# Performance work log

Measured on AMD Instinct MI355X. Metric: run time of the kernel, lower is better.

The kernel has to match this reference:

```python
import jax, jax.numpy as jnp
import numpy as np

N_LOC, N_EVT, E = 100000, 200000, 1000000
F_LOC, F_EVT, H = 128, 128, 64


def setup_inputs() -> dict:
    key = jax.random.key(0)
    ks = jax.random.split(key, 12)
    s = lambda k, shp: jax.random.normal(k, shp, dtype=jnp.float32) * (1.0 / np.sqrt(shp[0]))
    return {
        "loc_x": jax.random.normal(ks[0], (N_LOC, F_LOC), dtype=jnp.float32),
        "evt_x": jax.random.normal(ks[1], (N_EVT, F_EVT), dtype=jnp.float32),
        "edge_index": jax.random.randint(ks[2], (2, E), 0, N_LOC, dtype=jnp.int64),
        # projections (stored as (in, out))
        "W_loc": s(ks[3], (F_LOC, H)), "b_loc": jnp.zeros((H,), jnp.float32),
        "W_evt": s(ks[4], (F_EVT, H)), "b_evt": jnp.zeros((H,), jnp.float32),
        # SAGEConv: lin_l (on aggregated src, with bias), lin_r (on dst root, no bias)
        "W_l": s(ks[5], (H, H)), "b_l": jnp.zeros((H,), jnp.float32),
        "W_r": s(ks[6], (H, H)),
        # head MLP
        "W_h1": s(ks[7], (H, H // 2)), "b_h1": jnp.zeros((H // 2,), jnp.float32),
        "W_h2": s(ks[8], (H // 2, 1)), "b_h2": jnp.zeros((1,), jnp.float32),
    }


def reference(loc_x, evt_x, edge_index, W_loc, b_loc, W_evt, b_evt,
              W_l, b_l, W_r, W_h1, b_h1, W_h2, b_h2):
    # node projections + ReLU
    loc_h = jax.nn.relu(loc_x @ W_loc + b_loc)   # [N_loc, H]
    evt_h = jax.nn.relu(evt_x @ W_evt + b_evt)   # [N_evt, H]

    src, dst = edge_index[0], edge_index[1]      # event -> location
    n_loc = loc_h.shape[0]
    # mean aggregation of source (event) features onto destination (location) nodes
    msg_sum = jax.ops.segment_sum(evt_h[src], dst, num_segments=n_loc)   # [N_loc, H]
    cnt = jax.ops.segment_sum(jnp.ones_like(dst, dtype=loc_h.dtype), dst,
                              num_segments=n_loc)
    agg = msg_sum / jnp.maximum(cnt, 1.0)[:, None]
    # SAGEConv: lin_l(agg) + lin_r(root), then ReLU
    loc_h = jax.nn.relu(agg @ W_l + b_l + loc_h @ W_r)

    # prediction head
    h = jax.nn.relu(loc_h @ W_h1 + b_h1)
    logits = (h @ W_h2 + b_h2)[:, 0]             # [N_loc]
    return logits
```

## Files before the change

kernel.cpp:

```cpp
#include <hip/hip_runtime.h>


#define N_LOC 100000
#define N_EVT 200000
#define E_CNT 1000000
#define NTILES 6250
#define NBKT   256
#define BKT_L  391
#define CAPG   6000
#define QCAP   32
#define BKT_BLK 512
#define PERB   1954

#define PROJ_EVT_BLK 1536
#define PROJ_LOC_BLK 768
#define PROJ_BLK_TOT (PROJ_EVT_BLK + PROJ_LOC_BLK)
#define EVT_TILES 12500
#define LOC_TILES 6250
#define HEAD_BLK  1024

typedef __attribute__((ext_vector_type(8))) short short8;
typedef __attribute__((ext_vector_type(4))) float floatx4;
typedef __attribute__((ext_vector_type(8))) unsigned short ushort8v;

__device__ __forceinline__ float b2f(unsigned short u) {
    unsigned int x = ((unsigned int)u) << 16;
    return __builtin_bit_cast(float, x);
}
__device__ __forceinline__ unsigned short f2b(float f) {
    unsigned int x = __builtin_bit_cast(unsigned int, f);
    unsigned int r = (x + 0x7fffu + ((x >> 16) & 1u)) >> 16;
    return (unsigned short)r;
}
__device__ __forceinline__ float loadf(const void* p, int f32, size_t i) {
    return f32 ? ((const float*)p)[i] : b2f(((const unsigned short*)p)[i]);
}

__global__ __launch_bounds__(256) void prep_kernel(
    const void* t0, const void* t1, const int* eidx,
    const void* t3, const void* t4, const void* t5, const void* t6,
    const void* t7, const void* t8, const void* t9, const void* t10,
    const void* t11, const void* t12, const void* t13,
    int* flags, int* gbc, unsigned short* __restrict__ wp_all) {
    int b = blockIdx.x, tid = threadIdx.x;
    __shared__ int s0, s1;

    if (b == 14) { gbc[tid] = 0; return; }

    if (b >= 15) {
        int pb = b - 15;
        const void* W; int K, N, bstart, off;
        if (pb < 4)       { W = t5;  K = 128; N = 64; bstart = 0;  off = 0; }
        else if (pb < 8)  { W = t3;  K = 128; N = 64; bstart = 4;  off = 8192; }
        else if (pb < 10) { W = t7;  K = 64;  N = 64; bstart = 8;  off = 16384; }
        else if (pb < 12) { W = t9;  K = 64;  N = 64; bstart = 10; off = 20480; }
        else              { W = t10; K = 64;  N = 32; bstart = 12; off = 24576; }
        if (tid == 0) s0 = 0;
        __syncthreads();
        int nsamp = 2 * K * N; if (nsamp > 1024) nsamp = 1024;
        const unsigned short* h = (const unsigned short*)W;
        int susp = 0;
        for (int i = tid; i < nsamp; i += 256)
            if (((h[i] >> 7) & 0xFF) >= 0x90) susp++;
        if (susp) atomicAdd(&s0, susp);
        __syncthreads();
        int f32 = (s0 * 16 >= nsamp) ? 1 : 0;

        int idx  = (pb - bstart) * 256 + tid;
        int nk   = K >> 5;
        int f    = idx >> 6;
        int lane = idx & 63;
        int t  = f / nk;
        int kk = f - t * nk;
        int n  = t * 16 + (lane & 15);
        int k0 = kk * 32 + (lane >> 4) * 8;
        unsigned short tmp[8];
#pragma unroll
        for (int j = 0; j < 8; ++j) {
            size_t src = (size_t)(k0 + j) * N + n;
            tmp[j] = f32 ? f2b(((const float*)W)[src])
                         : ((const unsigned short*)W)[src];
        }
#pragma unroll
        for (int j = 0; j < 8; ++j) wp_all[(size_t)off + (size_t)idx * 8 + j] = tmp[j];
        return;
    }

    if (tid == 0) { s0 = 0; s1 = 0; }
    __syncthreads();
    if (b == 13) {
        if (tid < 128) {
            if (eidx[2 * tid] != 0) atomicAdd(&s0, 1);
            if (eidx[2 * tid + 1] != 0) atomicAdd(&s1, 1);
        }
        __syncthreads();
        if (tid == 0) flags[2] = (s1 == 0 && s0 > 32) ? 1 : 0;
        return;
    }
    const void* ptrs[13] = {t0, t1, t3, t4, t5, t6, t7, t8, t9, t10, t11, t12, t13};
    const int   cnts[13] = {12800000, 25600000, 8192, 64, 8192, 64,
                            4096, 64, 4096, 2048, 32, 32, 1};
    const int   slot[13] = {0, 1, 3, 4, 5, 6, 7, 8, 9, 10, 11, 12, 13};
    int nsamp = 2 * cnts[b];
    if (nsamp > 1024) nsamp = 1024;
    const unsigned short* h = (const unsigned short*)ptrs[b];
    int susp = 0;
    for (int i = tid; i < nsamp; i += 256)
        if (((h[i] >> 7) & 0xFF) >= 0x90) susp++;
    if (susp) atomicAdd(&s0, susp);
    __syncthreads();
    if (tid == 0) flags[slot[b]] = (s0 * 16 >= nsamp) ? 1 : 0;
}

__global__ __launch_bounds__(256, 3) void proj_both_kernel(
    const void* __restrict__ evt_x, const void* __restrict__ loc_x,
    const unsigned short* __restrict__ wp_all,
    const void* __restrict__ b_evt, const void* __restrict__ b_loc,
    unsigned short* __restrict__ evt_h, unsigned short* __restrict__ loc_h,
    const int* __restrict__ flags) {
    __shared__ unsigned short bs[8192];
    int blk = blockIdx.x;
    int tid = threadIdx.x, lane = tid & 63, wv = tid >> 6;
    int l15 = lane & 15, quad = lane >> 4;

    const void* X; const unsigned short* Wp; const void* bias;
    unsigned short* Y; int fx, fb, w0, nw, ntile;
    if (blk < PROJ_EVT_BLK) {
        X = evt_x; Wp = wp_all;        bias = b_evt; Y = evt_h;
        fx = flags[1]; fb = flags[6];
        w0 = blk * 4 + wv; nw = PROJ_EVT_BLK * 4; ntile = EVT_TILES;
    } else {
        X = loc_x; Wp = wp_all + 8192; bias = b_loc; Y = loc_h;
        fx = flags[0]; fb = flags[4];
        w0 = (blk - PROJ_EVT_BLK) * 4 + wv; nw = PROJ_LOC_BLK * 4; ntile = LOC_TILES;
    }

    {
        const short8* src = reinterpret_cast<const short8*>(Wp);
        short8* dst = reinterpret_cast<short8*>(bs);
#pragma unroll
        for (int i = 0; i < 4; ++i) dst[tid + i * 256] = src[tid + i * 256];
    }
    __syncthreads();

    float bv[4];
#pragma unroll
    for (int q = 0; q < 4; ++q) bv[q] = loadf(bias, fb, q * 16 + l15);

    if (w0 >= ntile) return;

    auto mfma_store = [&](const short8* a, int t) {
        floatx4 acc[4];
#pragma unroll
        for (int q = 0; q < 4; ++q) acc[q] = (floatx4)0.0f;
#pragma unroll
        for (int q = 0; q < 4; ++q) {
            short8 bq[4];
#pragma unroll
            for (int kk = 0; kk < 4; ++kk)
                bq[kk] = *reinterpret_cast<const short8*>(
                    &bs[((q * 4 + kk) * 64 + lane) * 8]);
#pragma unroll
            for (int kk = 0; kk < 4; ++kk)
                acc[q] = __builtin_amdgcn_mfma_f32_16x16x32_bf16(
                    a[kk], bq[kk], acc[q], 0, 0, 0);
        }
#pragma unroll
        for (int q = 0; q < 4; ++q)
#pragma unroll
            for (int r = 0; r < 4; ++r) {
                float v = acc[q][r] + bv[q];
                v = v > 0.0f ? v : 0.0f;
                Y[(size_t)(t * 16 + quad * 4 + r) * 64 + q * 16 + l15] = f2b(v);
            }
    };

    if (fx) {
        const float* Xf = (const float*)X;
        float4 pf[8];
        auto issueF = [&](int t) {
            const float* xr = Xf + (size_t)(t * 16 + l15) * 128 + quad * 8;
#pragma unroll
            for (int kk = 0; kk < 4; ++kk) {
                pf[kk * 2]     = *reinterpret_cast<const float4*>(xr + kk * 32);
                pf[kk * 2 + 1] = *reinterpret_cast<const float4*>(xr + kk * 32 + 4);
            }
        };
        issueF(w0);
        for (int t = w0; t < ntile; t += nw) {
            short8 a[4];
#pragma unroll
            for (int kk = 0; kk < 4; ++kk) {
                float4 p0 = pf[kk * 2], p1 = pf[kk * 2 + 1];
                short8 v;
                v[0] = (short)f2b(p0.x); v[1] = (short)f2b(p0.y);
                v[2] = (short)f2b(p0.z); v[3] = (short)f2b(p0.w);
                v[4] = (short)f2b(p1.x); v[5] = (short)f2b(p1.y);
                v[6] = (short)f2b(p1.z); v[7] = (short)f2b(p1.w);
                a[kk] = v;
            }
            int tn = t + nw;
            if (tn < ntile) issueF(tn);
            mfma_store(a, t);
        }
    } else {
        const unsigned short* Xh = (const unsigned short*)X;
        short8 an[4];
        auto issueH = [&](int t) {
            const unsigned short* xr = Xh + (size_t)(t * 16 + l15) * 128 + quad * 8;
#pragma unroll
            for (int kk = 0; kk < 4; ++kk)
                an[kk] = *reinterpret_cast<const short8*>(xr + kk * 32);
        };
        issueH(w0);
        for (int t = w0; t < ntile; t += nw) {
            short8 a[4];
#pragma unroll
            for (int kk = 0; kk < 4; ++kk) a[kk] = an[kk];
            int tn = t + nw;
            if (tn < ntile) issueH(tn);
            mfma_store(a, t);
        }
    }
}

__global__ __launch_bounds__(512) void bucket_kernel(
    const int* __restrict__ eidx, uint2* __restrict__ bkt,
    int* __restrict__ gbc, const int* __restrict__ flags) {
    __shared__ uint2 queue[NBKT][QCAP];
    __shared__ int qcnt[NBKT];
    int tid = threadIdx.x, blk = blockIdx.x;
    if (tid < NBKT) qcnt[tid] = 0;
    __syncthreads();
    int f64 = flags[2];
    const long long* e64 = (const long long*)eidx;
    int e0 = blk * PERB;
    int e1 = e0 + PERB; if (e1 > E_CNT) e1 = E_CNT;
    const int rounds = (PERB + 511) / 512;

    for (int r = 0; r < rounds; ++r) {
        int e = e0 + r * 512 + tid;
        if (e < e1) {
            int src, dst;
            if (f64) { src = (int)e64[e]; dst = (int)e64[E_CNT + e]; }
            else     { src = eidx[e];     dst = eidx[E_CNT + e]; }
            if ((unsigned)dst < (unsigned)N_LOC && (unsigned)src < (unsigned)N_EVT) {
                int bk = dst / BKT_L;
                int pos = atomicAdd(&qcnt[bk], 1);
                if (pos < QCAP) {
                    queue[bk][pos] = make_uint2((unsigned)src, (unsigned)dst);
                } else {
                    int p = atomicAdd(&gbc[bk], 1);
                    if (p < CAPG) bkt[(size_t)bk * CAPG + p] = make_uint2(src, dst);
                }
            }
        }
        __syncthreads();
        if (tid < NBKT) {
            int n = qcnt[tid]; if (n > QCAP) n = QCAP;
            while (n >= 16) {
                int gp = atomicAdd(&gbc[tid], 16);
                if (gp + 16 <= CAPG) {
                    uint2* d = bkt + (size_t)tid * CAPG + gp;
#pragma unroll
                    for (int j = 0; j < 16; ++j) d[j] = queue[tid][j];
                }
#pragma unroll
                for (int j = 16; j < QCAP; ++j) queue[tid][j - 16] = queue[tid][j];
                n -= 16;
            }
            qcnt[tid] = n;
        }
        __syncthreads();
    }
    if (tid < NBKT) {
        int n = qcnt[tid]; if (n > QCAP) n = QCAP;
        if (n > 0) {
            int gp = atomicAdd(&gbc[tid], n);
            for (int j = 0; j < n; ++j)
                if (gp + j < CAPG) bkt[(size_t)tid * CAPG + gp + j] = queue[tid][j];
        }
    }
}

__global__ __launch_bounds__(512) void csr_build_kernel(
    const uint2* __restrict__ bkt, const int* __restrict__ gbc,
    int* __restrict__ rowptr, int* __restrict__ csr) {
    __shared__ int sg[256];
    __shared__ int lcnt[512];
    __shared__ int lscan[512];
    __shared__ int lcsr[CAPG];
    int b = blockIdx.x, tid = threadIdx.x;
    int loc0 = b * BKT_L;
    int nloc = N_LOC - loc0; if (nloc > BKT_L) nloc = BKT_L;

    if (tid < 256) {
        int gv = gbc[tid]; if (gv > CAPG) gv = CAPG;
        sg[tid] = gv;
    }
    __syncthreads();
    for (int d = 1; d < 256; d <<= 1) {
        int x = (tid < 256 && tid >= d) ? sg[tid - d] : 0;
        __syncthreads();
        if (tid < 256) sg[tid] += x;
        __syncthreads();
    }
    int cntE = gbc[b]; if (cntE > CAPG) cntE = CAPG;
    int base = sg[b] - cntE;
    const uint2* bp = bkt + (size_t)b * CAPG;

    lcnt[tid] = 0;
    __syncthreads();
    for (int i = tid; i < cntE; i += 512) {
        int d = (int)bp[i].y - loc0;
        atomicAdd(&lcnt[d], 1);
    }
    __syncthreads();
    lscan[tid] = lcnt[tid];
    __syncthreads();
    for (int d = 1; d < 512; d <<= 1) {
        int v = (tid >= d) ? lscan[tid - d] : 0;
        __syncthreads();
        lscan[tid] += v;
        __syncthreads();
    }
    for (int i = tid; i < nloc; i += 512) {
        int excl = lscan[i] - lcnt[i];
        rowptr[loc0 + i] = base + excl;
        lcnt[i] = excl;
    }
    if (b == NBKT - 1 && tid == 0) rowptr[N_LOC] = base + cntE;
    __syncthreads();
    for (int i = tid; i < cntE; i += 512) {
        uint2 pr = bp[i];
        int d = (int)pr.y - loc0;
        int p = atomicAdd(&lcnt[d], 1);
        if (p < CAPG) lcsr[p] = (int)pr.x;
    }
    __syncthreads();
    for (int i = tid; i < cntE; i += 512) csr[base + i] = lcsr[i];
}

__global__ __launch_bounds__(256) void aggregate_kernel(
    const unsigned short* __restrict__ evt_h,
    const int* __restrict__ rowptr, const int* __restrict__ csr,
    unsigned short* __restrict__ agg, int N) {
    int wid  = (blockIdx.x * 256 + threadIdx.x) >> 6;
    int lane = threadIdx.x & 63;
    int eo = lane >> 3, cg = lane & 7;
    if (wid >= N) return;
    int e0 = rowptr[wid], e1 = rowptr[wid + 1];
    float a[8];
#pragma unroll
    for (int k = 0; k < 8; ++k) a[k] = 0.0f;

    int j = e0;
    for (; j + 16 <= e1; j += 16) {
        int s0 = csr[j + eo];
        int s1 = csr[j + 8 + eo];
        ushort8v v0 = *reinterpret_cast<const ushort8v*>(
            evt_h + (size_t)s0 * 64 + cg * 8);
        ushort8v v1 = *reinterpret_cast<const ushort8v*>(
            evt_h + (size_t)s1 * 64 + cg * 8);
#pragma unroll
        for (int k = 0; k < 8; ++k) a[k] += b2f(v0[k]) + b2f(v1[k]);
    }
    for (; j < e1; j += 8) {
        int jj = j + eo;
        bool c = jj < e1;
        int s = csr[c ? jj : j];
        ushort8v v = *reinterpret_cast<const ushort8v*>(
            evt_h + (size_t)s * 64 + cg * 8);
        if (c) {
#pragma unroll
            for (int k = 0; k < 8; ++k) a[k] += b2f(v[k]);
        }
    }
#pragma unroll
    for (int k = 0; k < 8; ++k) {
        a[k] += __shfl_xor(a[k], 8);
        a[k] += __shfl_xor(a[k], 16);
        a[k] += __shfl_xor(a[k], 32);
    }
    float inv = (e1 > e0) ? 1.0f / (float)(e1 - e0) : 0.0f;
    if (eo == 0) {
        ushort8v o;
#pragma unroll
        for (int k = 0; k < 8; ++k) o[k] = f2b(a[k] * inv);
        *reinterpret_cast<ushort8v*>(agg + (size_t)wid * 64 + cg * 8) = o;
    }
}

__global__ __launch_bounds__(256, 3) void head_kernel(
    const unsigned short* __restrict__ agg,
    const unsigned short* __restrict__ loc_h,
    const unsigned short* __restrict__ wp_all,
    const void* __restrict__ bl, const void* __restrict__ bh1,
    const void* __restrict__ wh2, const void* __restrict__ bh2,
    void* __restrict__ out, const int* __restrict__ flags) {
    __shared__ unsigned short bls[4096];
    __shared__ unsigned short brs[4096];
    __shared__ unsigned short b1s[2048];
    __shared__ unsigned short h2s[4][16 * 64];
    int tid = threadIdx.x, lane = tid & 63, wv = tid >> 6;
    int l15 = lane & 15, quad = lane >> 4;
    int fbl = flags[8], fbh1 = flags[11], fwh2 = flags[12], fbh2 = flags[13];
    int fout = flags[0];
    const unsigned short* wp_l  = wp_all + 16384;
    const unsigned short* wp_r  = wp_all + 20480;
    const unsigned short* wp_h1 = wp_all + 24576;

    {
        const short8* sl = reinterpret_cast<const short8*>(wp_l);
        const short8* sr = reinterpret_cast<const short8*>(wp_r);
        const short8* s1 = reinterpret_cast<const short8*>(wp_h1);
        short8* dl = reinterpret_cast<short8*>(bls);
        short8* dr = reinterpret_cast<short8*>(brs);
        short8* d1 = reinterpret_cast<short8*>(b1s);
        dl[tid] = sl[tid]; dl[tid + 256] = sl[tid + 256];
        dr[tid] = sr[tid]; dr[tid + 256] = sr[tid + 256];
        d1[tid] = s1[tid];
    }
    __syncthreads();

    float bbl[4], bh1v[2], w2v[2];
#pragma unroll
    for (int q = 0; q < 4; ++q) bbl[q] = loadf(bl, fbl, q * 16 + l15);
#pragma unroll
    for (int q = 0; q < 2; ++q) {
        bh1v[q] = loadf(bh1, fbh1, q * 16 + l15);
        w2v[q]  = loadf(wh2, fwh2, q * 16 + l15);
    }
    float bb2 = loadf(bh2, fbh2, 0);

    const int NW = HEAD_BLK * 4;
    int w0 = blockIdx.x * 4 + wv;
    if (w0 >= NTILES) return;

    short8 c0[4], c1[4];

    auto issue = [&](short8* c, int t) {
        int m = t * 16 + l15;
#pragma unroll
        for (int kk = 0; kk < 2; ++kk) {
            c[kk]     = *reinterpret_cast<const short8*>(
                agg + (size_t)m * 64 + kk * 32 + quad * 8);
            c[2 + kk] = *reinterpret_cast<const short8*>(
                loc_h + (size_t)m * 64 + kk * 32 + quad * 8);
        }
    };

    auto compute = [&](const short8* c, int tile) {
        floatx4 acc[4];
#pragma unroll
        for (int q = 0; q < 4; ++q) acc[q] = (floatx4)0.0f;
#pragma unroll
        for (int q = 0; q < 4; ++q) {
            short8 bwl[2], bwr[2];
#pragma unroll
            for (int kk = 0; kk < 2; ++kk) {
                bwl[kk] = *reinterpret_cast<const short8*>(
                    &bls[((q * 2 + kk) * 64 + lane) * 8]);
                bwr[kk] = *reinterpret_cast<const short8*>(
                    &brs[((q * 2 + kk) * 64 + lane) * 8]);
            }
#pragma unroll
            for (int kk = 0; kk < 2; ++kk) {
                acc[q] = __builtin_amdgcn_mfma_f32_16x16x32_bf16(
                    c[kk], bwl[kk], acc[q], 0, 0, 0);
                acc[q] = __builtin_amdgcn_mfma_f32_16x16x32_bf16(
                    c[2 + kk], bwr[kk], acc[q], 0, 0, 0);
            }
        }
#pragma unroll
        for (int q = 0; q < 4; ++q)
#pragma unroll
            for (int r = 0; r < 4; ++r) {
                float v = acc[q][r] + bbl[q];
                v = v > 0.0f ? v : 0.0f;
                h2s[wv][(quad * 4 + r) * 64 + q * 16 + l15] = f2b(v);
            }
        short8 aH[2];
#pragma unroll
        for (int kk = 0; kk < 2; ++kk)
            aH[kk] = *reinterpret_cast<const short8*>(
                &h2s[wv][l15 * 64 + kk * 32 + quad * 8]);

        floatx4 a1[2];
#pragma unroll
        for (int q = 0; q < 2; ++q) a1[q] = (floatx4)0.0f;
#pragma unroll
        for (int q = 0; q < 2; ++q) {
            short8 bw1[2];
#pragma unroll
            for (int kk = 0; kk < 2; ++kk)
                bw1[kk] = *reinterpret_cast<const short8*>(
                    &b1s[((q * 2 + kk) * 64 + lane) * 8]);
#pragma unroll
            for (int kk = 0; kk < 2; ++kk)
                a1[q] = __builtin_amdgcn_mfma_f32_16x16x32_bf16(
                    aH[kk], bw1[kk], a1[q], 0, 0, 0);
        }

        float s[4] = {0.f, 0.f, 0.f, 0.f};
#pragma unroll
        for (int q = 0; q < 2; ++q)
#pragma unroll
            for (int r = 0; r < 4; ++r) {
                float v = a1[q][r] + bh1v[q];
                v = v > 0.0f ? v : 0.0f;
                s[r] += v * w2v[q];
            }
#pragma unroll
        for (int r = 0; r < 4; ++r) {
            s[r] += __shfl_xor(s[r], 1);
            s[r] += __shfl_xor(s[r], 2);
            s[r] += __shfl_xor(s[r], 4);
            s[r] += __shfl_xor(s[r], 8);
        }
#pragma unroll
        for (int r = 0; r < 4; ++r) {
            if (l15 == r) {
                int row = tile * 16 + quad * 4 + r;
                float v = s[r] + bb2;
                if (fout) ((float*)out)[row] = v;
                else      ((unsigned short*)out)[row] = f2b(v);
            }
        }
    };

    issue(c0, w0);
    int t = w0;
    while (true) {
        int tn = t + NW;
        bool hn = tn < NTILES;
        if (hn) issue(c1, tn);
        compute(c0, t);
        if (!hn) break;
        t = tn; tn = t + NW; hn = tn < NTILES;
        if (hn) issue(c0, tn);
        compute(c1, t);
        if (!hn) break;
        t = tn;
    }
}

extern "C" void kernel_launch(void* const* d_in, const int* in_sizes, int n_in,
                              void* d_out, int out_size, void* d_ws, size_t ws_size,
                              hipStream_t stream) {
    (void)in_sizes; (void)n_in; (void)out_size; (void)ws_size;
    const void* loc_x = d_in[0];
    const void* evt_x = d_in[1];
    const int*  eidx  = (const int*)d_in[2];
    const void* W_loc = d_in[3];
    const void* b_loc = d_in[4];
    const void* W_evt = d_in[5];
    const void* b_evt = d_in[6];
    const void* W_l   = d_in[7];
    const void* b_l   = d_in[8];
    const void* W_r   = d_in[9];
    const void* W_h1  = d_in[10];
    const void* b_h1  = d_in[11];
    const void* W_h2  = d_in[12];
    const void* b_h2  = d_in[13];

    char* ws = (char*)d_ws;
    unsigned short* evt_h  = (unsigned short*)(ws);
    unsigned short* loc_h  = (unsigned short*)(ws + 25600000);
    int*            csr    = (int*)(ws + 38400000);
    int*            rowptr = (int*)(ws + 42400000);
    int*            gbc    = (int*)(ws + 42800016);
    unsigned short* wp_all = (unsigned short*)(ws + 42802064);
    int*            flags  = (int*)(ws + 42855312);
    uint2*          bkt    = (uint2*)(ws + 42855376);
    unsigned short* agg    = (unsigned short*)(ws + 42855376);

    prep_kernel<<<28, 256, 0, stream>>>(
        loc_x, evt_x, eidx, W_loc, b_loc, W_evt, b_evt,
        W_l, b_l, W_r, W_h1, b_h1, W_h2, b_h2,
        flags, gbc, wp_all);

    proj_both_kernel<<<PROJ_BLK_TOT, 256, 0, stream>>>(
        evt_x, loc_x, wp_all, b_evt, b_loc, evt_h, loc_h, flags);

    bucket_kernel<<<BKT_BLK, 512, 0, stream>>>(eidx, bkt, gbc, flags);
    csr_build_kernel<<<NBKT, 512, 0, stream>>>(bkt, gbc, rowptr, csr);

    aggregate_kernel<<<(N_LOC + 3) / 4, 256, 0, stream>>>(evt_h, rowptr, csr,
                                                          agg, N_LOC);

    head_kernel<<<HEAD_BLK, 256, 0, stream>>>(
        agg, loc_h, wp_all, b_l, b_h1, W_h2, b_h2, d_out, flags);
}
```

Baseline: 299.9 us.

## Fuse projection and edge bucketing into one interleaved kernel launch

Merges the node projection GEMM kernel and the edge bucketing kernel into a single launch. Blocks are interleaved 9 projection to 2 bucketing so that memory-bound scatter work overlaps with MFMA projection work, and one launch gap disappears. Bucketing blocks drop from 512 to 256 threads, and shared memory grows to the bucket queue size, reused as weight staging for projection blocks. The launch_bounds occupancy hint of 3 is removed, so the larger LDS footprint may lower occupancy of the projection path.

```diff
diff --git a/kernel.cpp b/kernel.cpp
--- a/kernel.cpp
+++ b/kernel.cpp
@@ -15,6 +15,7 @@
 #define PROJ_EVT_BLK 1536
 #define PROJ_LOC_BLK 768
 #define PROJ_BLK_TOT (PROJ_EVT_BLK + PROJ_LOC_BLK)
+#define PB_TOT (PROJ_BLK_TOT + BKT_BLK)
 #define EVT_TILES 12500
 #define LOC_TILES 6250
 #define HEAD_BLK  1024
@@ -112,15 +113,74 @@
     if (tid == 0) flags[slot[b]] = (s0 * 16 >= nsamp) ? 1 : 0;
 }
 
-__global__ __launch_bounds__(256, 3) void proj_both_kernel(
+__global__ __launch_bounds__(256) void proj_bucket_kernel(
     const void* __restrict__ evt_x, const void* __restrict__ loc_x,
     const unsigned short* __restrict__ wp_all,
     const void* __restrict__ b_evt, const void* __restrict__ b_loc,
     unsigned short* __restrict__ evt_h, unsigned short* __restrict__ loc_h,
-    const int* __restrict__ flags) {
-    __shared__ unsigned short bs[8192];
-    int blk = blockIdx.x;
-    int tid = threadIdx.x, lane = tid & 63, wv = tid >> 6;
+    const int* __restrict__ eidx, uint2* __restrict__ bkt,
+    int* __restrict__ gbc, const int* __restrict__ flags) {
+    __shared__ uint2 queue[NBKT][QCAP];
+    __shared__ int qcnt[NBKT];
+    int b = blockIdx.x;
+    int g = b / 11, r = b % 11;
+    int tid = threadIdx.x;
+
+    if (r >= 9) {
+        int blk = g * 2 + (r - 9);
+        qcnt[tid] = 0;
+        __syncthreads();
+        int f64 = flags[2];
+        const long long* e64 = (const long long*)eidx;
+        int e0 = blk * PERB;
+        int e1 = e0 + PERB; if (e1 > E_CNT) e1 = E_CNT;
+        const int rounds = (PERB + 255) / 256;
+
+        for (int rr = 0; rr < rounds; ++rr) {
+            int e = e0 + rr * 256 + tid;
+            if (e < e1) {
+                int src, dst;
+                if (f64) { src = (int)e64[e]; dst = (int)e64[E_CNT + e]; }
+                else     { src = eidx[e];     dst = eidx[E_CNT + e]; }
+                if ((unsigned)dst < (unsigned)N_LOC && (unsigned)src < (unsigned)N_EVT) {
+                    int bk = dst / BKT_L;
+                    int pos = atomicAdd(&qcnt[bk], 1);
+                    if (pos < QCAP) {
+                        queue[bk][pos] = make_uint2((unsigned)src, (unsigned)dst);
+                    } else {
+                        int p = atomicAdd(&gbc[bk], 1);
+                        if (p < CAPG) bkt[(size_t)bk * CAPG + p] = make_uint2(src, dst);
+                    }
+                }
+            }
+            __syncthreads();
+            int n = qcnt[tid]; if (n > QCAP) n = QCAP;
+            while (n >= 16) {
+                int gp = atomicAdd(&gbc[tid], 16);
+                if (gp + 16 <= CAPG) {
+                    uint2* d = bkt + (size_t)tid * CAPG + gp;
+#pragma unroll
+                    for (int j = 0; j < 16; ++j) d[j] = queue[tid][j];
+                }
+#pragma unroll
+                for (int j = 16; j < QCAP; ++j) queue[tid][j - 16] = queue[tid][j];
+                n -= 16;
+            }
+            qcnt[tid] = n;
+            __syncthreads();
+        }
+        int n = qcnt[tid]; if (n > QCAP) n = QCAP;
+        if (n > 0) {
+            int gp = atomicAdd(&gbc[tid], n);
+            for (int j = 0; j < n; ++j)
+                if (gp + j < CAPG) bkt[(size_t)tid * CAPG + gp + j] = queue[tid][j];
+        }
+        return;
+    }
+
+    unsigned short* bs = (unsigned short*)&queue[0][0];
+    int blk = g * 9 + r;
+    int lane = tid & 63, wv = tid >> 6;
     int l15 = lane & 15, quad = lane >> 4;
 
     const void* X; const unsigned short* Wp; const void* bias;
@@ -168,10 +228,10 @@
 #pragma unroll
         for (int q = 0; q < 4; ++q)
 #pragma unroll
-            for (int r = 0; r < 4; ++r) {
-                float v = acc[q][r] + bv[q];
+            for (int rr = 0; rr < 4; ++rr) {
+                float v = acc[q][rr] + bv[q];
                 v = v > 0.0f ? v : 0.0f;
-                Y[(size_t)(t * 16 + quad * 4 + r) * 64 + q * 16 + l15] = f2b(v);
+                Y[(size_t)(t * 16 + quad * 4 + rr) * 64 + q * 16 + l15] = f2b(v);
             }
     };
 
@@ -220,65 +280,6 @@
             int tn = t + nw;
             if (tn < ntile) issueH(tn);
             mfma_store(a, t);
-        }
-    }
-}
-
-__global__ __launch_bounds__(512) void bucket_kernel(
-    const int* __restrict__ eidx, uint2* __restrict__ bkt,
-    int* __restrict__ gbc, const int* __restrict__ flags) {
-    __shared__ uint2 queue[NBKT][QCAP];
-    __shared__ int qcnt[NBKT];
-    int tid = threadIdx.x, blk = blockIdx.x;
-    if (tid < NBKT) qcnt[tid] = 0;
-    __syncthreads();
-    int f64 = flags[2];
-    const long long* e64 = (const long long*)eidx;
-    int e0 = blk * PERB;
-    int e1 = e0 + PERB; if (e1 > E_CNT) e1 = E_CNT;
-    const int rounds = (PERB + 511) / 512;
-
-    for (int r = 0; r < rounds; ++r) {
-        int e = e0 + r * 512 + tid;
-        if (e < e1) {
-            int src, dst;
-            if (f64) { src = (int)e64[e]; dst = (int)e64[E_CNT + e]; }
-            else     { src = eidx[e];     dst = eidx[E_CNT + e]; }
-            if ((unsigned)dst < (unsigned)N_LOC && (unsigned)src < (unsigned)N_EVT) {
-                int bk = dst / BKT_L;
-                int pos = atomicAdd(&qcnt[bk], 1);
-                if (pos < QCAP) {
-                    queue[bk][pos] = make_uint2((unsigned)src, (unsigned)dst);
-                } else {
-                    int p = atomicAdd(&gbc[bk], 1);
-                    if (p < CAPG) bkt[(size_t)bk * CAPG + p] = make_uint2(src, dst);
-                }
-            }
-        }
-        __syncthreads();
-        if (tid < NBKT) {
-            int n = qcnt[tid]; if (n > QCAP) n = QCAP;
-            while (n >= 16) {
-                int gp = atomicAdd(&gbc[tid], 16);
-                if (gp + 16 <= CAPG) {
-                    uint2* d = bkt + (size_t)tid * CAPG + gp;
-#pragma unroll
-                    for (int j = 0; j < 16; ++j) d[j] = queue[tid][j];
-                }
-#pragma unroll
-                for (int j = 16; j < QCAP; ++j) queue[tid][j - 16] = queue[tid][j];
-                n -= 16;
-            }
-            qcnt[tid] = n;
-        }
-        __syncthreads();
-    }
-    if (tid < NBKT) {
-        int n = qcnt[tid]; if (n > QCAP) n = QCAP;
-        if (n > 0) {
-            int gp = atomicAdd(&gbc[tid], n);
-            for (int j = 0; j < n; ++j)
-                if (gp + j < CAPG) bkt[(size_t)tid * CAPG + gp + j] = queue[tid][j];
         }
     }
 }
@@ -475,10 +476,10 @@
 #pragma unroll
         for (int q = 0; q < 4; ++q)
 #pragma unroll
-            for (int r = 0; r < 4; ++r) {
-                float v = acc[q][r] + bbl[q];
+            for (int rr = 0; rr < 4; ++rr) {
+                float v = acc[q][rr] + bbl[q];
                 v = v > 0.0f ? v : 0.0f;
-                h2s[wv][(quad * 4 + r) * 64 + q * 16 + l15] = f2b(v);
+                h2s[wv][(quad * 4 + rr) * 64 + q * 16 + l15] = f2b(v);
             }
         short8 aH[2];
 #pragma unroll
@@ -506,23 +507,23 @@
 #pragma unroll
         for (int q = 0; q < 2; ++q)
 #pragma unroll
-            for (int r = 0; r < 4; ++r) {
-                float v = a1[q][r] + bh1v[q];
+            for (int rr = 0; rr < 4; ++rr) {
+                float v = a1[q][rr] + bh1v[q];
                 v = v > 0.0f ? v : 0.0f;
-                s[r] += v * w2v[q];
-            }
-#pragma unroll
-        for (int r = 0; r < 4; ++r) {
-            s[r] += __shfl_xor(s[r], 1);
-            s[r] += __shfl_xor(s[r], 2);
-            s[r] += __shfl_xor(s[r], 4);
-            s[r] += __shfl_xor(s[r], 8);
-        }
-#pragma unroll
-        for (int r = 0; r < 4; ++r) {
-            if (l15 == r) {
-                int row = tile * 16 + quad * 4 + r;
-                float v = s[r] + bb2;
+                s[rr] += v * w2v[q];
+            }
+#pragma unroll
+        for (int rr = 0; rr < 4; ++rr) {
+            s[rr] += __shfl_xor(s[rr], 1);
+            s[rr] += __shfl_xor(s[rr], 2);
+            s[rr] += __shfl_xor(s[rr], 4);
+            s[rr] += __shfl_xor(s[rr], 8);
+        }
+#pragma unroll
+        for (int rr = 0; rr < 4; ++rr) {
+            if (l15 == rr) {
+                int row = tile * 16 + quad * 4 + rr;
+                float v = s[rr] + bb2;
                 if (fout) ((float*)out)[row] = v;
                 else      ((unsigned short*)out)[row] = f2b(v);
             }
@@ -580,10 +581,10 @@
         W_l, b_l, W_r, W_h1, b_h1, W_h2, b_h2,
         flags, gbc, wp_all);
 
-    proj_both_kernel<<<PROJ_BLK_TOT, 256, 0, stream>>>(
-        evt_x, loc_x, wp_all, b_evt, b_loc, evt_h, loc_h, flags);
-
-    bucket_kernel<<<BKT_BLK, 512, 0, stream>>>(eidx, bkt, gbc, flags);
+    proj_bucket_kernel<<<PB_TOT, 256, 0, stream>>>(
+        evt_x, loc_x, wp_all, b_evt, b_loc, evt_h, loc_h,
+        eidx, bkt, gbc, flags);
+
     csr_build_kernel<<<NBKT, 512, 0, stream>>>(bkt, gbc, rowptr, csr);
 
     aggregate_kernel<<<(N_LOC + 3) / 4, 256, 0, stream>>>(evt_h, rowptr, csr,
```

After: 288.0 us, median of 2. 1.04x faster.
